# Performance work log

Hardware: AMD Instinct MI355X
Metric: run time of the kernel (lower is better)

Reference implementation:

```python
import jax, jax.numpy as jnp
import numpy as np

ALPHA = 0.2  # LeakyReLU negative slope
NEG_INF = -1e9


def setup_inputs() -> dict:
    key = jax.random.key(0)
    k1, k2, k3, k4 = jax.random.split(key, 4)
    B, N, Fin, Fout = 8, 2048, 128, 64
    h = jax.random.normal(k1, (B, N, Fin), dtype=jnp.float32)
    adj_mask = jax.random.randint(k2, (B, N, N), 0, 2).astype(jnp.int32)
    # xavier_uniform-style scales
    W = jax.random.uniform(k3, (Fout, Fin), dtype=jnp.float32,
                           minval=-1.0, maxval=1.0) * np.sqrt(6.0 / (Fin + Fout))
    a = jax.random.uniform(k4, (2 * Fout,), dtype=jnp.float32,
                           minval=-1.0, maxval=1.0) * np.sqrt(6.0 / (2 * Fout + 1))
    return {"h": h, "adj_mask": adj_mask, "W": W, "a": a}


def reference(h, adj_mask, W, a):
    # Wh: [B, N, Fout]
    Wh = jnp.einsum("bnf,of->bno", h, W)
    Fout = Wh.shape[-1]
    a1, a2 = a[:Fout], a[Fout:]
    # additive decomposition of a([Wh_i || Wh_j]): e_ij = leakyrelu(s1_i + s2_j)
    s1 = Wh @ a1  # [B, N]
    s2 = Wh @ a2  # [B, N]
    e = jax.nn.leaky_relu(s1[:, :, None] + s2[:, None, :], negative_slope=ALPHA)  # [B,N,N]
    e = jnp.where(adj_mask == 0, NEG_INF, e)
    attention = jax.nn.softmax(e, axis=-1)
    # dropout is identity in eval mode / p effectively 0 for the reference
    h_prime = jnp.einsum("bij,bjo->bio", attention, Wh)
    return h_prime
```

## Files before the change

### kernel.cpp

```cpp
#include <hip/hip_runtime.h>
#include <hip/hip_fp16.h>
#include <math.h>

#define LRELU_ALPHA 0.2f

constexpr int B_ = 8, N_ = 2048, FIN = 128, FOUT = 64;

typedef _Float16 f16x2 __attribute__((ext_vector_type(2)));
typedef _Float16 f16x8 __attribute__((ext_vector_type(8)));
typedef float f32x4 __attribute__((ext_vector_type(4)));

__device__ __forceinline__ unsigned short f2h(float x) {
  return __half_as_ushort(__float2half(x));
}

__global__ __launch_bounds__(256) void k_pack(const int* __restrict__ adj,
                                              unsigned int* __restrict__ bits) {
  const size_t g = (size_t)blockIdx.x * 256 + threadIdx.x;
  const int4* src = (const int4*)adj + g * 8;
  int4 v[8];
#pragma unroll
  for (int c = 0; c < 8; ++c) v[c] = src[c];
  unsigned int w = 0;
#pragma unroll
  for (int c = 0; c < 8; ++c) {
    w |= (v[c].x != 0 ? 1u : 0u) << (c * 4 + 0);
    w |= (v[c].y != 0 ? 1u : 0u) << (c * 4 + 1);
    w |= (v[c].z != 0 ? 1u : 0u) << (c * 4 + 2);
    w |= (v[c].w != 0 ? 1u : 0u) << (c * 4 + 3);
  }
  bits[g] = w;
}

__global__ __launch_bounds__(256) void k_wh(
    const float* __restrict__ h, const float* __restrict__ W,
    const float* __restrict__ a, unsigned short* __restrict__ WhT,
    ushort4* __restrict__ e1th, unsigned int* __restrict__ e2h2) {
  __shared__ float Wt[128][65];
  __shared__ float hs[16][128];

  const int t = threadIdx.x;
  const int row0 = blockIdx.x * 16;

  for (int e = t; e < 64 * 128; e += 256) {
    int o = e >> 7, f = e & 127;
    Wt[f][o] = W[e];
  }
  {
    const float4* hg = (const float4*)(h + (size_t)row0 * FIN);
    for (int i4 = t; i4 < 16 * 32; i4 += 256) {
      int r = i4 >> 5, f4 = i4 & 31;
      *(float4*)&hs[r][f4 * 4] = hg[i4];
    }
  }
  __syncthreads();

  const int wave = t >> 6, lane = t & 63;
  float acc[4] = {0.f, 0.f, 0.f, 0.f};
#pragma unroll 4
  for (int f4 = 0; f4 < 32; ++f4) {
    float w0 = Wt[4 * f4 + 0][lane], w1 = Wt[4 * f4 + 1][lane];
    float w2 = Wt[4 * f4 + 2][lane], w3 = Wt[4 * f4 + 3][lane];
#pragma unroll
    for (int r = 0; r < 4; ++r) {
      float4 hv = *(const float4*)&hs[wave * 4 + r][f4 * 4];
      acc[r] += hv.x * w0 + hv.y * w1 + hv.z * w2 + hv.w * w3;
    }
  }

  const float a1v = a[lane], a2v = a[64 + lane];
  const int b = row0 / N_;
#pragma unroll
  for (int r = 0; r < 4; ++r) {
    const int row = row0 + wave * 4 + r;
    const int n = row - b * N_;
    const float v = acc[r];
    WhT[((size_t)b * 64 + lane) * N_ + n] = f2h(v);
    float p1 = v * a1v, p2 = v * a2v;
#pragma unroll
    for (int d = 32; d; d >>= 1) {
      p1 += __shfl_xor(p1, d, 64);
      p2 += __shfl_xor(p2, d, 64);
    }
    if (lane == 0) {
      ushort4 e1;
      e1.x = f2h(__expf(p1 - 1.0f));
      e1.y = f2h(__expf(LRELU_ALPHA * p1 - 1.0f));
      e1.z = f2h(__expf(-1.0f - p1));
      e1.w = 0;
      e1th[row] = e1;
      e2h2[row] = (unsigned int)f2h(__expf(p2 - 1.0f)) |
                  ((unsigned int)f2h(__expf(LRELU_ALPHA * p2 - 1.0f)) << 16);
    }
  }
}

__global__ __launch_bounds__(256, 2) void k_attn(
    const unsigned short* __restrict__ WhT,
    const ushort4* __restrict__ e1th, const unsigned int* __restrict__ e2h2,
    const unsigned int* __restrict__ bits,
    float* __restrict__ pa, float* __restrict__ ls) {
  __shared__ __align__(16) unsigned short whs[64 * 256];
  __shared__ unsigned int e2s[256];
  __shared__ float accm[4][64][20];

  const int t = threadIdx.x;
  const int wv = t >> 6, lane = t & 63;
  const int m = lane & 15, q = lane >> 4;
  const int ir = blockIdx.x, jw = blockIdx.y, b = blockIdx.z;
  const int i0 = ir * 256, jw0 = jw * 256;

  const unsigned short* whB = WhT + (size_t)b * 64 * N_ + jw0;
#pragma unroll
  for (int l = 0; l < 8; ++l) {
    int id = l * 256 + t;
    int o = id >> 5, c = id & 31;
    uint4 v = *(const uint4*)(whB + (size_t)o * N_ + c * 8);
    int sc = c ^ (o & 31);
    *(uint4*)&whs[o * 256 + sc * 8] = v;
  }
  e2s[t] = e2h2[b * N_ + jw0 + t];
  __syncthreads();

  int boff[2][4];
#pragma unroll
  for (int ks = 0; ks < 2; ++ks)
#pragma unroll
    for (int g = 0; g < 4; ++g) {
      int o = g * 16 + m;
      int c = wv * 8 + ks * 4 + q;
      boff[ks][g] = o * 512 + ((c ^ (o & 31)) << 4);
    }
  const int e2base0 = wv * 64 + q * 8;

  const f16x8 ones = {1, 1, 1, 1, 1, 1, 1, 1};

#pragma unroll 1
  for (int it = 0; it < 16; ++it) {
    const int row = i0 + it * 16 + m;
    const ushort4 e1u = e1th[b * N_ + row];
    const uint2 w2 =
        *(const uint2*)(bits + ((size_t)(b * N_ + row)) * 64 + jw * 8 + wv * 2);
    const f16x2 e1p2 = __builtin_bit_cast(
        f16x2, (unsigned int)e1u.x | ((unsigned int)e1u.y << 16));
    const _Float16 Tf = __builtin_bit_cast(_Float16, (unsigned short)e1u.z);

    f32x4 ac0 = {0.f, 0.f, 0.f, 0.f}, ac1 = ac0, ac2 = ac0, ac3 = ac0, lf = ac0;

#pragma unroll
    for (int ks = 0; ks < 2; ++ks) {
      const unsigned int word = (ks ? w2.y : w2.x) >> (q * 8);
      const uint4* ep = (const uint4*)&e2s[e2base0 + ks * 32];
      const uint4 E0 = ep[0], E1v = ep[1];
      const unsigned int eu[8] = {E0.x, E0.y, E0.z, E0.w,
                                  E1v.x, E1v.y, E1v.z, E1v.w};
      f16x8 af;
#pragma unroll
      for (int jj = 0; jj < 8; ++jj) {
        f16x2 e2p = __builtin_bit_cast(f16x2, eu[jj]);
        f16x2 pr = e1p2 * e2p;
        _Float16 ps = (e2p.x > Tf) ? pr.x : pr.y;
        ps = ((word >> jj) & 1u) ? ps : (_Float16)0.0f;
        af[jj] = ps;
      }
      f16x8 b0 = *(const f16x8*)((const char*)whs + boff[ks][0]);
      f16x8 b1 = *(const f16x8*)((const char*)whs + boff[ks][1]);
      f16x8 b2 = *(const f16x8*)((const char*)whs + boff[ks][2]);
      f16x8 b3 = *(const f16x8*)((const char*)whs + boff[ks][3]);
      ac0 = __builtin_amdgcn_mfma_f32_16x16x32_f16(af, b0, ac0, 0, 0, 0);
      ac1 = __builtin_amdgcn_mfma_f32_16x16x32_f16(af, b1, ac1, 0, 0, 0);
      ac2 = __builtin_amdgcn_mfma_f32_16x16x32_f16(af, b2, ac2, 0, 0, 0);
      ac3 = __builtin_amdgcn_mfma_f32_16x16x32_f16(af, b3, ac3, 0, 0, 0);
      lf  = __builtin_amdgcn_mfma_f32_16x16x32_f16(af, ones, lf, 0, 0, 0);
    }

    {
      float* al = &accm[wv][lane][0];
      *(f32x4*)(al + 0) = ac0;
      *(f32x4*)(al + 4) = ac1;
      *(f32x4*)(al + 8) = ac2;
      *(f32x4*)(al + 12) = ac3;
      *(f32x4*)(al + 16) = lf;
    }
    __syncthreads();
    {
      const int ri = t >> 4, c4 = t & 15;
      const int g = c4 >> 2, qq = ri >> 2, rr = ri & 3;
      float4 s = {0.f, 0.f, 0.f, 0.f};
#pragma unroll
      for (int w = 0; w < 4; ++w) {
        const int lbase = qq * 16 + (c4 & 3) * 4;
        s.x += accm[w][lbase + 0][g * 4 + rr];
        s.y += accm[w][lbase + 1][g * 4 + rr];
        s.z += accm[w][lbase + 2][g * 4 + rr];
        s.w += accm[w][lbase + 3][g * 4 + rr];
      }
      const size_t oidx = (size_t)jw * 1048576 +
                          ((size_t)(b * N_ + i0 + it * 16 + ri)) * 64 + c4 * 4;
      *(float4*)&pa[oidx] = s;
      if (t < 16) {
        float l = 0.f;
#pragma unroll
        for (int w = 0; w < 4; ++w) l += accm[w][(t >> 2) * 16][16 + (t & 3)];
        ls[jw * 16384 + b * N_ + i0 + it * 16 + t] = l;
      }
    }
    __syncthreads();
  }
}

__global__ __launch_bounds__(256) void k_reduce(const float* __restrict__ pa,
                                                const float* __restrict__ ls,
                                                float* __restrict__ out) {
  const size_t e = (size_t)blockIdx.x * 256 + threadIdx.x;
  const int ifl = (int)(e >> 6);
  float s = 0.f, l = 0.f;
#pragma unroll
  for (int jw = 0; jw < 8; ++jw) {
    s += pa[(size_t)jw * 1048576 + e];
    l += ls[jw * 16384 + ifl];
  }
  out[e] = s / (l == 0.f ? 1.f : l);
}

extern "C" void kernel_launch(void* const* d_in, const int* in_sizes, int n_in,
                              void* d_out, int out_size, void* d_ws, size_t ws_size,
                              hipStream_t stream) {
  const float* h   = (const float*)d_in[0];
  const int*   adj = (const int*)d_in[1];
  const float* W   = (const float*)d_in[2];
  const float* a   = (const float*)d_in[3];
  float* out = (float*)d_out;

  unsigned short* WhT = (unsigned short*)d_ws;
  ushort4* e1th = (ushort4*)(WhT + (size_t)B_ * 64 * N_);
  unsigned int* e2h2 = (unsigned int*)(e1th + B_ * N_);
  unsigned int* bits = (unsigned int*)(e2h2 + B_ * N_);
  float* pa = (float*)(bits + (size_t)B_ * N_ * (N_ / 32));
  float* ls = pa + (size_t)8 * 1048576;

  const int nwords = B_ * N_ * (N_ / 32);
  k_pack<<<dim3(nwords / 256), 256, 0, stream>>>(adj, bits);
  k_wh<<<dim3(B_ * N_ / 16), 256, 0, stream>>>(h, W, a, WhT, e1th, e2h2);
  k_attn<<<dim3(8, 8, 8), 256, 0, stream>>>(WhT, e1th, e2h2, bits, pa, ls);
  k_reduce<<<dim3(4096), 256, 0, stream>>>(pa, ls, out);
}
```

Baseline: 244.4 us.

## Split k_attn work across waves by rows instead of columns, drop LDS cross-wave reduction

Each wave now owns 64 rows and walks the full 256-column tile, so per-row partial sums no longer need to go through shared memory with two block barriers per 16-row step. The leaky-ReLU branch select is replaced by a max of the positive and negative exp products, which removes the threshold value and the compare against it. The e2 factors are stored as separate half arrays. In exchange each thread holds many more accumulator registers (16 tiles plus 4 row-sum vectors), which may limit occupancy, and output stores become scalar rather than float4.

```diff
diff --git a/kernel.cpp b/kernel.cpp
--- a/kernel.cpp
+++ b/kernel.cpp
@@ -35,7 +35,8 @@
 __global__ __launch_bounds__(256) void k_wh(
     const float* __restrict__ h, const float* __restrict__ W,
     const float* __restrict__ a, unsigned short* __restrict__ WhT,
-    ushort4* __restrict__ e1th, unsigned int* __restrict__ e2h2) {
+    unsigned int* __restrict__ e1h2, unsigned short* __restrict__ e2ps,
+    unsigned short* __restrict__ e2ns) {
   __shared__ float Wt[128][65];
   __shared__ float hs[16][128];
 
@@ -83,26 +84,23 @@
       p2 += __shfl_xor(p2, d, 64);
     }
     if (lane == 0) {
-      ushort4 e1;
-      e1.x = f2h(__expf(p1 - 1.0f));
-      e1.y = f2h(__expf(LRELU_ALPHA * p1 - 1.0f));
-      e1.z = f2h(__expf(-1.0f - p1));
-      e1.w = 0;
-      e1th[row] = e1;
-      e2h2[row] = (unsigned int)f2h(__expf(p2 - 1.0f)) |
-                  ((unsigned int)f2h(__expf(LRELU_ALPHA * p2 - 1.0f)) << 16);
+      e1h2[row] = (unsigned int)f2h(__expf(p1 - 1.0f)) |
+                  ((unsigned int)f2h(__expf(LRELU_ALPHA * p1 - 1.0f)) << 16);
+      e2ps[row] = f2h(__expf(p2 - 1.0f));
+      e2ns[row] = f2h(__expf(LRELU_ALPHA * p2 - 1.0f));
     }
   }
 }
 
 __global__ __launch_bounds__(256, 2) void k_attn(
     const unsigned short* __restrict__ WhT,
-    const ushort4* __restrict__ e1th, const unsigned int* __restrict__ e2h2,
+    const unsigned int* __restrict__ e1h2,
+    const unsigned short* __restrict__ e2ps,
+    const unsigned short* __restrict__ e2ns,
     const unsigned int* __restrict__ bits,
     float* __restrict__ pa, float* __restrict__ ls) {
   __shared__ __align__(16) unsigned short whs[64 * 256];
-  __shared__ unsigned int e2s[256];
-  __shared__ float accm[4][64][20];
+  __shared__ __align__(16) unsigned short e2sp[256], e2sn[256];
 
   const int t = threadIdx.x;
   const int wv = t >> 6, lane = t & 63;
@@ -110,102 +108,88 @@
   const int ir = blockIdx.x, jw = blockIdx.y, b = blockIdx.z;
   const int i0 = ir * 256, jw0 = jw * 256;
 
+  unsigned int e1u[4];
+  uint4 wA[4], wB[4];
+#pragma unroll
+  for (int tt = 0; tt < 4; ++tt) {
+    const int row = b * N_ + i0 + wv * 64 + tt * 16 + m;
+    e1u[tt] = e1h2[row];
+    const uint4* bp = (const uint4*)(bits + (size_t)row * 64 + jw * 8);
+    wA[tt] = bp[0];
+    wB[tt] = bp[1];
+  }
+
   const unsigned short* whB = WhT + (size_t)b * 64 * N_ + jw0;
 #pragma unroll
   for (int l = 0; l < 8; ++l) {
     int id = l * 256 + t;
     int o = id >> 5, c = id & 31;
     uint4 v = *(const uint4*)(whB + (size_t)o * N_ + c * 8);
-    int sc = c ^ (o & 31);
-    *(uint4*)&whs[o * 256 + sc * 8] = v;
-  }
-  e2s[t] = e2h2[b * N_ + jw0 + t];
+    *(uint4*)&whs[o * 256 + ((c ^ (o & 31)) << 3)] = v;
+  }
+  e2sp[t] = e2ps[b * N_ + jw0 + t];
+  e2sn[t] = e2ns[b * N_ + jw0 + t];
   __syncthreads();
 
-  int boff[2][4];
-#pragma unroll
-  for (int ks = 0; ks < 2; ++ks)
+  f32x4 acc[4][4];
+  f32x4 lf[4];
+#pragma unroll
+  for (int tt = 0; tt < 4; ++tt) {
+    lf[tt] = (f32x4){0.f, 0.f, 0.f, 0.f};
+#pragma unroll
+    for (int g = 0; g < 4; ++g) acc[tt][g] = (f32x4){0.f, 0.f, 0.f, 0.f};
+  }
+
+  const f16x8 ones = {1, 1, 1, 1, 1, 1, 1, 1};
+  const int qb = q * 8;
+
+#pragma unroll
+  for (int ks = 0; ks < 8; ++ks) {
+    f16x8 bfr[4];
 #pragma unroll
     for (int g = 0; g < 4; ++g) {
-      int o = g * 16 + m;
-      int c = wv * 8 + ks * 4 + q;
-      boff[ks][g] = o * 512 + ((c ^ (o & 31)) << 4);
-    }
-  const int e2base0 = wv * 64 + q * 8;
-
-  const f16x8 ones = {1, 1, 1, 1, 1, 1, 1, 1};
-
-#pragma unroll 1
-  for (int it = 0; it < 16; ++it) {
-    const int row = i0 + it * 16 + m;
-    const ushort4 e1u = e1th[b * N_ + row];
-    const uint2 w2 =
-        *(const uint2*)(bits + ((size_t)(b * N_ + row)) * 64 + jw * 8 + wv * 2);
-    const f16x2 e1p2 = __builtin_bit_cast(
-        f16x2, (unsigned int)e1u.x | ((unsigned int)e1u.y << 16));
-    const _Float16 Tf = __builtin_bit_cast(_Float16, (unsigned short)e1u.z);
-
-    f32x4 ac0 = {0.f, 0.f, 0.f, 0.f}, ac1 = ac0, ac2 = ac0, ac3 = ac0, lf = ac0;
-
-#pragma unroll
-    for (int ks = 0; ks < 2; ++ks) {
-      const unsigned int word = (ks ? w2.y : w2.x) >> (q * 8);
-      const uint4* ep = (const uint4*)&e2s[e2base0 + ks * 32];
-      const uint4 E0 = ep[0], E1v = ep[1];
-      const unsigned int eu[8] = {E0.x, E0.y, E0.z, E0.w,
-                                  E1v.x, E1v.y, E1v.z, E1v.w};
+      const int o = g * 16 + m;
+      bfr[g] = *(const f16x8*)&whs[o * 256 + (((ks * 4 + q) ^ (o & 31)) << 3)];
+    }
+    const f16x8 e2pv = *(const f16x8*)&e2sp[ks * 32 + qb];
+    const f16x8 e2nv = *(const f16x8*)&e2sn[ks * 32 + qb];
+
+#pragma unroll
+    for (int tt = 0; tt < 4; ++tt) {
+      const uint4 wq4 = (ks < 4) ? wA[tt] : wB[tt];
+      const unsigned int word =
+          (ks & 3) == 0 ? wq4.x : (ks & 3) == 1 ? wq4.y
+                        : (ks & 3) == 2 ? wq4.z : wq4.w;
+      const unsigned int wq = word >> qb;
+      const f16x2 e1 = __builtin_bit_cast(f16x2, e1u[tt]);
       f16x8 af;
 #pragma unroll
       for (int jj = 0; jj < 8; ++jj) {
-        f16x2 e2p = __builtin_bit_cast(f16x2, eu[jj]);
-        f16x2 pr = e1p2 * e2p;
-        _Float16 ps = (e2p.x > Tf) ? pr.x : pr.y;
-        ps = ((word >> jj) & 1u) ? ps : (_Float16)0.0f;
-        af[jj] = ps;
+        _Float16 pp = e1.x * e2pv[jj];
+        _Float16 pn = e1.y * e2nv[jj];
+        _Float16 pm = pp > pn ? pp : pn;
+        af[jj] = ((wq >> jj) & 1u) ? pm : (_Float16)0;
       }
-      f16x8 b0 = *(const f16x8*)((const char*)whs + boff[ks][0]);
-      f16x8 b1 = *(const f16x8*)((const char*)whs + boff[ks][1]);
-      f16x8 b2 = *(const f16x8*)((const char*)whs + boff[ks][2]);
-      f16x8 b3 = *(const f16x8*)((const char*)whs + boff[ks][3]);
-      ac0 = __builtin_amdgcn_mfma_f32_16x16x32_f16(af, b0, ac0, 0, 0, 0);
-      ac1 = __builtin_amdgcn_mfma_f32_16x16x32_f16(af, b1, ac1, 0, 0, 0);
-      ac2 = __builtin_amdgcn_mfma_f32_16x16x32_f16(af, b2, ac2, 0, 0, 0);
-      ac3 = __builtin_amdgcn_mfma_f32_16x16x32_f16(af, b3, ac3, 0, 0, 0);
-      lf  = __builtin_amdgcn_mfma_f32_16x16x32_f16(af, ones, lf, 0, 0, 0);
-    }
-
-    {
-      float* al = &accm[wv][lane][0];
-      *(f32x4*)(al + 0) = ac0;
-      *(f32x4*)(al + 4) = ac1;
-      *(f32x4*)(al + 8) = ac2;
-      *(f32x4*)(al + 12) = ac3;
-      *(f32x4*)(al + 16) = lf;
-    }
-    __syncthreads();
-    {
-      const int ri = t >> 4, c4 = t & 15;
-      const int g = c4 >> 2, qq = ri >> 2, rr = ri & 3;
-      float4 s = {0.f, 0.f, 0.f, 0.f};
-#pragma unroll
-      for (int w = 0; w < 4; ++w) {
-        const int lbase = qq * 16 + (c4 & 3) * 4;
-        s.x += accm[w][lbase + 0][g * 4 + rr];
-        s.y += accm[w][lbase + 1][g * 4 + rr];
-        s.z += accm[w][lbase + 2][g * 4 + rr];
-        s.w += accm[w][lbase + 3][g * 4 + rr];
-      }
-      const size_t oidx = (size_t)jw * 1048576 +
-                          ((size_t)(b * N_ + i0 + it * 16 + ri)) * 64 + c4 * 4;
-      *(float4*)&pa[oidx] = s;
-      if (t < 16) {
-        float l = 0.f;
-#pragma unroll
-        for (int w = 0; w < 4; ++w) l += accm[w][(t >> 2) * 16][16 + (t & 3)];
-        ls[jw * 16384 + b * N_ + i0 + it * 16 + t] = l;
-      }
-    }
-    __syncthreads();
+      acc[tt][0] = __builtin_amdgcn_mfma_f32_16x16x32_f16(af, bfr[0], acc[tt][0], 0, 0, 0);
+      acc[tt][1] = __builtin_amdgcn_mfma_f32_16x16x32_f16(af, bfr[1], acc[tt][1], 0, 0, 0);
+      acc[tt][2] = __builtin_amdgcn_mfma_f32_16x16x32_f16(af, bfr[2], acc[tt][2], 0, 0, 0);
+      acc[tt][3] = __builtin_amdgcn_mfma_f32_16x16x32_f16(af, bfr[3], acc[tt][3], 0, 0, 0);
+      lf[tt] = __builtin_amdgcn_mfma_f32_16x16x32_f16(af, ones, lf[tt], 0, 0, 0);
+    }
+  }
+
+#pragma unroll
+  for (int tt = 0; tt < 4; ++tt) {
+    const int rowb = i0 + wv * 64 + tt * 16;
+#pragma unroll
+    for (int r = 0; r < 4; ++r) {
+      const size_t off = (size_t)jw * 1048576 +
+                         ((size_t)(b * N_ + rowb + q * 4 + r)) * 64;
+#pragma unroll
+      for (int g = 0; g < 4; ++g) pa[off + g * 16 + m] = acc[tt][g][r];
+      if (m == 0)
+        ls[jw * 16384 + b * N_ + rowb + q * 4 + r] = lf[tt][r];
+    }
   }
 }
 
@@ -233,15 +217,16 @@
   float* out = (float*)d_out;
 
   unsigned short* WhT = (unsigned short*)d_ws;
-  ushort4* e1th = (ushort4*)(WhT + (size_t)B_ * 64 * N_);
-  unsigned int* e2h2 = (unsigned int*)(e1th + B_ * N_);
-  unsigned int* bits = (unsigned int*)(e2h2 + B_ * N_);
+  unsigned int* e1h2 = (unsigned int*)(WhT + (size_t)B_ * 64 * N_);
+  unsigned short* e2ps = (unsigned short*)(e1h2 + B_ * N_);
+  unsigned short* e2ns = e2ps + B_ * N_;
+  unsigned int* bits = (unsigned int*)(e2ns + B_ * N_);
   float* pa = (float*)(bits + (size_t)B_ * N_ * (N_ / 32));
   float* ls = pa + (size_t)8 * 1048576;
 
   const int nwords = B_ * N_ * (N_ / 32);
   k_pack<<<dim3(nwords / 256), 256, 0, stream>>>(adj, bits);
-  k_wh<<<dim3(B_ * N_ / 16), 256, 0, stream>>>(h, W, a, WhT, e1th, e2h2);
-  k_attn<<<dim3(8, 8, 8), 256, 0, stream>>>(WhT, e1th, e2h2, bits, pa, ls);
+  k_wh<<<dim3(B_ * N_ / 16), 256, 0, stream>>>(h, W, a, WhT, e1h2, e2ps, e2ns);
+  k_attn<<<dim3(8, 8, 8), 256, 0, stream>>>(WhT, e1h2, e2ps, e2ns, bits, pa, ls);
   k_reduce<<<dim3(4096), 256, 0, stream>>>(pa, ls, out);
 }
```

New measurement: 238.9 us. 2.2% less time.
